# Kernel optimization log

Measured on AMD Instinct MI355X. Metric: run time of the kernel, lower is better.

## Reference

```python
import jax, jax.numpy as jnp
import numpy as np

B, T, H = 64, 512, 256
D = 2 * H            # input dim to slot LSTM (bidirectional encoder repr)
MAX_SLOTS = 64       # max slot spans kept per sentence
MAX_LEN = 8          # max tokens per span
N_SLOT_TYPES = 64


def _pack_spans(bio):
    """Segment BIO tags into spans: each span = B token + following I tokens.
    Returns token index table [B, MAX_SLOTS, MAX_LEN] and validity mask."""
    bsz, t = bio.shape
    bmask = bio == 1
    imask = bio == 2
    sid = jnp.cumsum(bmask.astype(jnp.int32), axis=1) - 1      # span id per token
    valid = (bmask | imask) & (sid >= 0)
    cs = jnp.cumsum(valid.astype(jnp.int32), axis=1)           # running count of span tokens
    bi = jnp.arange(bsz)[:, None]
    # cs value at each span's B token (overflow spans dumped into slot MAX_SLOTS)
    sid_b = jnp.where(bmask & (sid < MAX_SLOTS), sid, MAX_SLOTS)
    start = jnp.zeros((bsz, MAX_SLOTS + 1), jnp.int32).at[bi, sid_b].set(cs)[:, :MAX_SLOTS]
    sid_c = jnp.clip(sid, 0, MAX_SLOTS - 1)
    rank = cs - jnp.take_along_axis(start, sid_c, axis=1)      # position within span (B token -> 0)
    ok = valid & (sid < MAX_SLOTS) & (rank < MAX_LEN)
    s_idx = jnp.where(ok, sid_c, MAX_SLOTS)
    r_idx = jnp.where(ok, rank, MAX_LEN)
    tpos = jnp.broadcast_to(jnp.arange(t, dtype=jnp.int32), (bsz, t))
    tok = jnp.zeros((bsz, MAX_SLOTS + 1, MAX_LEN + 1), jnp.int32).at[bi, s_idx, r_idx].set(tpos)
    vm = jnp.zeros((bsz, MAX_SLOTS + 1, MAX_LEN + 1), bool).at[bi, s_idx, r_idx].set(True)
    return tok[:, :MAX_SLOTS, :MAX_LEN], vm[:, :MAX_SLOTS, :MAX_LEN]


def _lstm(x, Wih, Whh, b):
    """Unidirectional LSTM. x: [N, L, D] -> outputs [N, L, H] (torch gate order i,f,g,o)."""
    xg = jnp.einsum('nld,gd->nlg', x, Wih) + b                 # [N, L, 4H]
    n, l, _ = xg.shape
    h0 = jnp.zeros((n, Whh.shape[1]), x.dtype)

    def step(carry, xt):
        h, c = carry
        g = xt + h @ Whh.T
        i, f, gg, o = jnp.split(g, 4, axis=-1)
        c = jax.nn.sigmoid(f) * c + jax.nn.sigmoid(i) * jnp.tanh(gg)
        h = jax.nn.sigmoid(o) * jnp.tanh(c)
        return (h, c), h

    _, hs = jax.lax.scan(step, (h0, h0), jnp.swapaxes(xg, 0, 1))
    return jnp.swapaxes(hs, 0, 1)


def reference(lstm_repr, W_ih_f, W_hh_f, b_f, W_ih_b, W_hh_b, b_b, slot_emb, bio):
    tok, vm = _pack_spans(bio)                                  # [B,MS,ML], [B,MS,ML]
    bi = jnp.arange(lstm_repr.shape[0])[:, None, None]
    spans = lstm_repr[bi, tok]                                  # [B,MS,ML,D]
    lens = vm.sum(-1)                                           # [B,MS]
    # reverse each span within its valid length (padding stays at the end)
    pos = jnp.arange(MAX_LEN)
    rpos = lens[..., None] - 1 - pos
    ridx = jnp.where(rpos >= 0, rpos, 0)
    spans_rev = jnp.take_along_axis(spans, ridx[..., None], axis=2)
    ms = MAX_SLOTS
    xf = spans.reshape(-1, MAX_LEN, D)
    xb = spans_rev.reshape(-1, MAX_LEN, D)
    m = vm.reshape(-1, MAX_LEN, 1).astype(lstm_repr.dtype)
    hf = _lstm(xf, W_ih_f, W_hh_f, b_f)                         # [B*MS, ML, H]
    hb = _lstm(xb, W_ih_b, W_hh_b, b_b)
    pooled = jnp.concatenate([(hf * m).sum(1), (hb * m).sum(1)], axis=-1)  # sum-pool over span
    pooled = pooled.reshape(lstm_repr.shape[0], ms, 2 * H)
    scores = jnp.einsum('bsh,kh->bsk', pooled, slot_emb)        # [B,MS,n_slot_types]
    scores = scores * (lens > 0)[..., None]
    return scores


def setup_inputs() -> dict:
    key = jax.random.key(0)
    ks = jax.random.split(key, 9)
    s = 0.05
    return {
        'lstm_repr': jax.random.normal(ks[0], (B, T, D), jnp.float32),
        'W_ih_f': jax.random.normal(ks[1], (4 * H, D), jnp.float32) * s,
        'W_hh_f': jax.random.normal(ks[2], (4 * H, H), jnp.float32) * s,
        'b_f': jax.random.normal(ks[3], (4 * H,), jnp.float32) * s,
        'W_ih_b': jax.random.normal(ks[4], (4 * H, D), jnp.float32) * s,
        'W_hh_b': jax.random.normal(ks[5], (4 * H, H), jnp.float32) * s,
        'b_b': jax.random.normal(ks[6], (4 * H,), jnp.float32) * s,
        'slot_emb': jax.random.normal(ks[7], (N_SLOT_TYPES, 2 * H), jnp.float32) * s,
        'bio': jax.random.randint(ks[8], (B, T), 0, 3, dtype=jnp.int32),
    }
```

## Files before the change

### kernel.cpp

```cpp
#include <hip/hip_runtime.h>
#include <hip/hip_bf16.h>
#include <stdint.h>

#define B_ 64
#define T_ 512
#define H_ 256
#define D_ 512
#define MS_ 64
#define ML_ 8
#define NST_ 64

typedef unsigned short u16;
typedef __bf16 bf8 __attribute__((ext_vector_type(8)));
typedef float f4 __attribute__((ext_vector_type(4)));

__device__ __forceinline__ u16 f2bf(float f) {
    unsigned u = __builtin_bit_cast(unsigned, f);
    u += 0x7fffu + ((u >> 16) & 1u);
    return (u16)(u >> 16);
}
__device__ __forceinline__ float bf2f(u16 v) {
    return __builtin_bit_cast(float, (unsigned)v << 16);
}
__device__ __forceinline__ float sigm(float x) { return 1.f / (1.f + __expf(-x)); }


__global__ __launch_bounds__(512) void pack_spans2(const int* __restrict__ bio,
                                                   int* __restrict__ tok,
                                                   int* __restrict__ lenb) {
    __shared__ int wsum[8];
    __shared__ int start_s[64];
    __shared__ int len_s[64];
    int b = blockIdx.x;
    int t = threadIdx.x;
    int lane = t & 63, w = t >> 6;
    int v = bio[b * T_ + t];
    int bm = (v == 1);
    int im = (v == 2);
    if (t < 64) len_s[t] = 0;

    int x = bm;
#pragma unroll
    for (int off = 1; off < 64; off <<= 1) {
        int y = __shfl_up(x, off, 64);
        if (lane >= off) x += y;
    }
    if (lane == 63) wsum[w] = x;
    __syncthreads();
    int wof = 0;
    for (int i = 0; i < w; ++i) wof += wsum[i];
    int sid = x + wof - 1;
    int valid = ((bm | im) && sid >= 0) ? 1 : 0;
    __syncthreads();

    x = valid;
#pragma unroll
    for (int off = 1; off < 64; off <<= 1) {
        int y = __shfl_up(x, off, 64);
        if (lane >= off) x += y;
    }
    if (lane == 63) wsum[w] = x;
    __syncthreads();
    wof = 0;
    for (int i = 0; i < w; ++i) wof += wsum[i];
    int cs = x + wof;

    if (bm && sid < MS_) start_s[sid] = cs;
    __syncthreads();

    if (valid && sid < MS_) {
        int rank = cs - start_s[sid];
        if (rank < ML_) {
            tok[(b * MS_ + sid) * ML_ + rank] = t;
            atomicAdd(&len_s[sid], 1);
        }
    }
    __syncthreads();
    if (t < 64) lenb[b * MS_ + t] = len_s[t];
}

__global__ __launch_bounds__(256) void prep(
        const float* __restrict__ wihf, const float* __restrict__ whhf,
        const float* __restrict__ wihb, const float* __restrict__ whhb,
        const float* __restrict__ bf, const float* __restrict__ bb,
        u16* __restrict__ wcx, u16* __restrict__ wch, float* __restrict__ bc,
        const float* __restrict__ repr, const int* __restrict__ tok,
        const int* __restrict__ lenb,
        int* __restrict__ lists, int* __restrict__ counts, u16* __restrict__ xg) {
    int bid = blockIdx.x, gsz = gridDim.x, tid = threadIdx.x;
    if (bid == 0) {
        __shared__ int wsum[4];
        int lane = tid & 63, w = tid >> 6;
        int len[16];
#pragma unroll
        for (int i = 0; i < 16; ++i) len[i] = lenb[tid * 16 + i];
        for (int p = 0; p < ML_; ++p) {
            int c = 0;
#pragma unroll
            for (int i = 0; i < 16; ++i) c += (len[i] > p) ? 1 : 0;
            int x = c;
#pragma unroll
            for (int off = 1; off < 64; off <<= 1) {
                int y = __shfl_up(x, off, 64);
                if (lane >= off) x += y;
            }
            if (lane == 63) wsum[w] = x;
            __syncthreads();
            int wof = 0;
            for (int i = 0; i < w; ++i) wof += wsum[i];
            int pos = wof + x - c;
#pragma unroll
            for (int i = 0; i < 16; ++i)
                if (len[i] > p) lists[p * 4096 + pos++] = tid * 16 + i;
            if (tid == 255) counts[p] = pos;
            __syncthreads();
        }
        return;
    }
    int b1 = bid - 1, g1 = gsz - 1;
    for (int ch = b1; ch < 6152; ch += g1) {
        int i = ch * 256 + tid;
        if (i < 1572864) {
            int dir = i / 786432;
            int rem = i - dir * 786432;
            int n = rem / 768;
            int k = rem - n * 768;
            int nn = n & 63, c = n >> 6;
            int orig = (nn >> 4) * 256 + c * 16 + (nn & 15);
            if (k < 512) {
                const float* wih = dir ? wihb : wihf;
                wcx[((size_t)dir * 1024 + n) * 512 + k] = f2bf(wih[orig * 512 + k]);
            } else {
                const float* whh = dir ? whhb : whhf;
                wch[((size_t)dir * 1024 + n) * 256 + (k - 512)] =
                    f2bf(whh[orig * 256 + (k - 512)]);
            }
        } else if (i < 1574912) {
            int i2 = i - 1572864;
            int dir = i2 >> 10;
            int n = i2 & 1023;
            int nn = n & 63, c = n >> 6;
            int orig = (nn >> 4) * 256 + c * 16 + (nn & 15);
            bc[i2] = (dir ? bb : bf)[orig];
        }
    }
    for (int gq = b1; gq < 8192; gq += g1) {
        int sr = gq * 4 + (tid >> 6);
        int i = tid & 63;
        int span = sr >> 3, rank = sr & 7;
        if (rank < lenb[span]) {
            int t = tok[sr];
            int b = span >> 6;
            const float4* src = (const float4*)(repr + (size_t)(b * T_ + t) * D_);
            ushort4* dst = (ushort4*)(xg + (size_t)sr * D_);
            float4 v0 = src[i * 2], v1 = src[i * 2 + 1];
            ushort4 o0, o1;
            o0.x = f2bf(v0.x); o0.y = f2bf(v0.y); o0.z = f2bf(v0.z); o0.w = f2bf(v0.w);
            o1.x = f2bf(v1.x); o1.y = f2bf(v1.y); o1.z = f2bf(v1.z); o1.w = f2bf(v1.w);
            dst[i * 2] = o0; dst[i * 2 + 1] = o1;
        }
    }
}

__global__ __launch_bounds__(256) void xgk(const u16* __restrict__ xg,
                                           const u16* __restrict__ wcx,
                                           const float* __restrict__ bc,
                                           const int* __restrict__ lenb,
                                           const int* __restrict__ lists,
                                           const int* __restrict__ counts,
                                           u16* __restrict__ xgates,
                                           float* __restrict__ cbuf,
                                           u16* __restrict__ h1,
                                           float* __restrict__ pooled) {
    __shared__ __align__(16) u16 As[64 * 72];
    __shared__ __align__(16) u16 Bs[64 * 72];
    __shared__ unsigned xoffs[64];
    __shared__ int spans_s[64];
    int tid = threadIdx.x;
    int lane = tid & 63;
    int w16 = (tid >> 6) * 16;
    int mr = lane & 15;
    int q = lane >> 4;
    int q8 = q * 8;

    int S = 0;
#pragma unroll
    for (int pp = 0; pp < 8; ++pp) S += (counts[pp] + 63) >> 6;
    int S2 = 2 * S;

    int it = blockIdx.x;
    int qq = it >> 7, rem = it & 127, xs = rem >> 3, r8 = rem & 7;
    int g = qq * 8 + r8;
    if (g >= S2) return;
    int dir = (g >= S) ? 1 : 0;
    int gg = dir ? g - S : g;
    int p = 0;
#pragma unroll
    for (int pp = 0; pp < 7; ++pp) {
        int nbp = (counts[pp] + 63) >> 6;
        bool adv = (p == pp) && (gg >= nbp);
        if (adv) { gg -= nbp; p = pp + 1; }
    }
    int rbk = gg;
    int cnt = counts[p];
    int base = rbk * 64;

    if (tid < 64) {
        unsigned xo = 0;
        int span = 0;
        int idx = base + tid;
        if (idx < cnt) {
            span = lists[p * 4096 + idx];
            int L = lenb[span];
            int rank = dir ? (L - 1 - p) : p;
            xo = (unsigned)(span * ML_ + rank) * D_;
        }
        xoffs[tid] = xo;
        spans_s[tid] = span;
    }
    __syncthreads();

    int n0 = xs * 64;
    const u16* wb = wcx + (size_t)dir * 1024 * 512;
    f4 acc[4];
    f4 zed = {0.f, 0.f, 0.f, 0.f};
#pragma unroll
    for (int i = 0; i < 4; ++i) acc[i] = zed;

    for (int kt = 0; kt < 8; ++kt) {
#pragma unroll
        for (int i = 0; i < 2; ++i) {
            int c = tid + i * 256;
            int row = c >> 3;
            int cc = (c & 7) * 8;
            *(uint4*)&As[row * 72 + cc] =
                *(const uint4*)(xg + xoffs[row] + kt * 64 + cc);
            *(uint4*)&Bs[row * 72 + cc] =
                *(const uint4*)(wb + (size_t)(n0 + row) * 512 + kt * 64 + cc);
        }
        __syncthreads();
#pragma unroll
        for (int kk = 0; kk < 64; kk += 32) {
            bf8 af = *(const bf8*)&As[(w16 + mr) * 72 + kk + q8];
#pragma unroll
            for (int nt = 0; nt < 4; ++nt) {
                bf8 bg = *(const bf8*)&Bs[(nt * 16 + mr) * 72 + kk + q8];
                acc[nt] = __builtin_amdgcn_mfma_f32_16x16x32_bf16(af, bg, acc[nt], 0, 0, 0);
            }
        }
        __syncthreads();
    }

    float tf[16];
#pragma unroll
    for (int nt = 0; nt < 4; ++nt)
#pragma unroll
        for (int r = 0; r < 4; ++r) {
            int n = n0 + nt * 16 + mr;
            tf[nt * 4 + r] = acc[nt][r] + bc[dir * 1024 + n];
        }

    if (p == 0) {
        int j = xs * 16 + mr;
#pragma unroll
        for (int r = 0; r < 4; ++r) {
            int m = w16 + q * 4 + r;
            if (base + m < cnt) {
                int span = spans_s[m];
                float gi = tf[0 + r], gg2 = tf[8 + r], go = tf[12 + r];
                float cn = sigm(gi) * tanhf(gg2);
                float h = sigm(go) * tanhf(cn);
                int si = (dir * 4096 + span) * H_ + j;
                cbuf[si] = cn;
                h1[si] = f2bf(h);
                pooled[span * 512 + dir * H_ + j] = h;
            }
        }
    } else {
        int y = (dir * 8 + p) * 64 + rbk;
        u16 tmp[16];
#pragma unroll
        for (int i = 0; i < 16; ++i) tmp[i] = f2bf(tf[i]);
        size_t off = ((size_t)(y * 16 + xs) * 256 + tid) * 16;
        *(uint4*)&xgates[off] = *(const uint4*)tmp;
        *(uint4*)&xgates[off + 8] = *(const uint4*)(tmp + 8);
    }
}

__global__ __launch_bounds__(256) void stepk(const u16* __restrict__ xgates,
                                             const u16* __restrict__ hin,
                                             u16* __restrict__ hout,
                                             const u16* __restrict__ wch,
                                             const int* __restrict__ lists,
                                             const int* __restrict__ counts,
                                             float* __restrict__ cbuf,
                                             float* __restrict__ pooled, int p) {
    __shared__ __align__(16) u16 As[64 * 264];
    __shared__ __align__(16) u16 Bs[64 * 264];
    __shared__ unsigned hoffs[64];
    __shared__ int spans_s[64];
    int tid = threadIdx.x;
    int lane = tid & 63;
    int w16 = (tid >> 6) * 16;
    int mr = lane & 15;
    int q = lane >> 4;
    int q8 = q * 8;
    int cnt = counts[p];
    int nbp = (cnt + 63) >> 6;
    int S2 = 2 * nbp;

    int it = blockIdx.x;
    int g = it >> 4, xs = it & 15;
    if (g >= S2) return;
    int dir = (g >= nbp) ? 1 : 0;
    int rbk = dir ? g - nbp : g;
    int base = rbk * 64;

    if (tid < 64) {
        int span = 0;
        int idx = base + tid;
        if (idx < cnt) span = lists[p * 4096 + idx];
        spans_s[tid] = span;
        hoffs[tid] = (unsigned)(dir * 4096 + span) * H_;
    }
    __syncthreads();

    int n0 = xs * 64;
    const u16* wb = wch + (size_t)dir * 1024 * 256;
    int y = (dir * 8 + p) * 64 + rbk;
    u16 tmp[16];
    {
        const uint4* sx = (const uint4*)(xgates + ((size_t)(y * 16 + xs) * 256 + tid) * 16);
        ((uint4*)tmp)[0] = sx[0];
        ((uint4*)tmp)[1] = sx[1];
    }
    f4 acc[4];
#pragma unroll
    for (int nt = 0; nt < 4; ++nt)
#pragma unroll
        for (int r = 0; r < 4; ++r) acc[nt][r] = bf2f(tmp[nt * 4 + r]);

#pragma unroll
    for (int i = 0; i < 8; ++i) {
        int c = tid + i * 256;
        int row = c >> 5;
        int cc = (c & 31) * 8;
        *(uint4*)&As[row * 264 + cc] = *(const uint4*)(hin + hoffs[row] + cc);
        *(uint4*)&Bs[row * 264 + cc] =
            *(const uint4*)(wb + (size_t)(n0 + row) * 256 + cc);
    }
    __syncthreads();

#pragma unroll
    for (int kk = 0; kk < 256; kk += 32) {
        bf8 af = *(const bf8*)&As[(w16 + mr) * 264 + kk + q8];
#pragma unroll
        for (int nt = 0; nt < 4; ++nt) {
            bf8 bg = *(const bf8*)&Bs[(nt * 16 + mr) * 264 + kk + q8];
            acc[nt] = __builtin_amdgcn_mfma_f32_16x16x32_bf16(af, bg, acc[nt], 0, 0, 0);
        }
    }

#pragma unroll
    for (int r = 0; r < 4; ++r) {
        int m = w16 + q * 4 + r;
        if (base + m < cnt) {
            int span = spans_s[m];
            int j = xs * 16 + mr;
            float gi = acc[0][r], gf = acc[1][r], gg = acc[2][r], go = acc[3][r];
            int si = (dir * 4096 + span) * H_ + j;
            float c = cbuf[si];
            float cn = sigm(gf) * c + sigm(gi) * tanhf(gg);
            float h = sigm(go) * tanhf(cn);
            cbuf[si] = cn;
            hout[si] = f2bf(h);
            pooled[span * 512 + dir * H_ + j] += h;
        }
    }
}

__global__ __launch_bounds__(256) void scoresk(const float* __restrict__ pooled,
                                               const float* __restrict__ emb,
                                               const int* __restrict__ lenb,
                                               float* __restrict__ out) {
    __shared__ __align__(16) u16 As[64 * 72];
    __shared__ __align__(16) u16 Bs[64 * 72];
    int g = blockIdx.x;
    int tid = threadIdx.x;
    int lane = tid & 63;
    int w16 = (tid >> 6) * 16;
    int mr = lane & 15;
    int q = lane >> 4;
    int q8 = q * 8;

    f4 acc[4];
    f4 zed = {0.f, 0.f, 0.f, 0.f};
#pragma unroll
    for (int i = 0; i < 4; ++i) acc[i] = zed;

    for (int kt = 0; kt < 8; ++kt) {
#pragma unroll
        for (int i = 0; i < 2; ++i) {
            int c = tid + i * 256;
            int row = c >> 3;
            int cc = (c & 7) * 8;
            const float4* a =
                (const float4*)(pooled + (size_t)(g * 64 + row) * 512 + kt * 64 + cc);
            float4 v0 = a[0], v1 = a[1];
            ushort4 o0, o1;
            o0.x = f2bf(v0.x); o0.y = f2bf(v0.y); o0.z = f2bf(v0.z); o0.w = f2bf(v0.w);
            o1.x = f2bf(v1.x); o1.y = f2bf(v1.y); o1.z = f2bf(v1.z); o1.w = f2bf(v1.w);
            *(ushort4*)&As[row * 72 + cc] = o0;
            *(ushort4*)&As[row * 72 + cc + 4] = o1;
            const float4* b = (const float4*)(emb + (size_t)row * 512 + kt * 64 + cc);
            float4 w0 = b[0], w1 = b[1];
            ushort4 p0, p1;
            p0.x = f2bf(w0.x); p0.y = f2bf(w0.y); p0.z = f2bf(w0.z); p0.w = f2bf(w0.w);
            p1.x = f2bf(w1.x); p1.y = f2bf(w1.y); p1.z = f2bf(w1.z); p1.w = f2bf(w1.w);
            *(ushort4*)&Bs[row * 72 + cc] = p0;
            *(ushort4*)&Bs[row * 72 + cc + 4] = p1;
        }
        __syncthreads();
#pragma unroll
        for (int kk = 0; kk < 64; kk += 32) {
            bf8 af = *(const bf8*)&As[(w16 + mr) * 72 + kk + q8];
#pragma unroll
            for (int nt = 0; nt < 4; ++nt) {
                bf8 bg = *(const bf8*)&Bs[(nt * 16 + mr) * 72 + kk + q8];
                acc[nt] = __builtin_amdgcn_mfma_f32_16x16x32_bf16(af, bg, acc[nt], 0, 0, 0);
            }
        }
        __syncthreads();
    }

#pragma unroll
    for (int r = 0; r < 4; ++r) {
        int m = g * 64 + w16 + q * 4 + r;
        int ln = lenb[m];
#pragma unroll
        for (int nt = 0; nt < 4; ++nt) {
            int n = nt * 16 + mr;
            out[(size_t)m * 64 + n] = (ln > 0) ? acc[nt][r] : 0.f;
        }
    }
}


extern "C" void kernel_launch(void* const* d_in, const int* in_sizes, int n_in,
                              void* d_out, int out_size, void* d_ws, size_t ws_size,
                              hipStream_t stream) {
    const float* lstm_repr = (const float*)d_in[0];
    const float* W_ih_f = (const float*)d_in[1];
    const float* W_hh_f = (const float*)d_in[2];
    const float* b_f    = (const float*)d_in[3];
    const float* W_ih_b = (const float*)d_in[4];
    const float* W_hh_b = (const float*)d_in[5];
    const float* b_b    = (const float*)d_in[6];
    const float* slot_emb = (const float*)d_in[7];
    const int* bio      = (const int*)d_in[8];
    float* out = (float*)d_out;

    char* ws = (char*)d_ws;
    u16*  xg     = (u16*)(ws + 0);
    u16*  xgates = (u16*)(ws + 33554432);
    u16*  wcx    = (u16*)(ws + 167772160);
    u16*  wch    = (u16*)(ws + 169869312);
    float* bc    = (float*)(ws + 170917888);
    int*  tok    = (int*)(ws + 170926080);
    int*  lenb   = (int*)(ws + 171057152);
    int*  lists  = (int*)(ws + 171073536);
    int*  counts = (int*)(ws + 171204608);
    float* pooled= (float*)(ws + 171204864);
    float* cbuf  = (float*)(ws + 179593472);
    u16*  h0     = (u16*)(ws + 187982080);
    u16*  h1     = (u16*)(ws + 192176384);

    pack_spans2<<<64, 512, 0, stream>>>(bio, tok, lenb);
    prep<<<2048, 256, 0, stream>>>(W_ih_f, W_hh_f, W_ih_b, W_hh_b, b_f, b_b,
                                   wcx, wch, bc, lstm_repr, tok, lenb,
                                   lists, counts, xg);
    xgk<<<16384, 256, 0, stream>>>(xg, wcx, bc, lenb, lists, counts, xgates,
                                   cbuf, h1, pooled);
    for (int p = 1; p < 8; ++p) {
        const u16* hin = (p & 1) ? h1 : h0;
        u16* hout = (p & 1) ? h0 : h1;
        stepk<<<2048, 256, 0, stream>>>(xgates, hin, hout, wch, lists, counts,
                                        cbuf, pooled, p);
    }
    scoresk<<<64, 256, 0, stream>>>(pooled, slot_emb, lenb, out);
}
```

Baseline: 243.3 us.

## Fuse seven recurrent step launches into one persistent kernel with length-sorted spans

Spans are now sorted by descending length into one master list, so every timestep's active set is a prefix of that list. The seven per-step launches are replaced by a single kernel of 128 blocks. Each block owns 64 spans and one direction, keeps h in LDS across steps, and loops over all 16 gate column slices, double-buffering the W_hh tiles. This removes the launch overhead and the global round trips for h, but the grid shrinks from 2048 blocks to 128, so parallelism drops and each block reloads all of W_hh at every step.

```diff
diff --git a/kernel.cpp b/kernel.cpp
--- a/kernel.cpp
+++ b/kernel.cpp
@@ -86,7 +86,7 @@
         u16* __restrict__ wcx, u16* __restrict__ wch, float* __restrict__ bc,
         const float* __restrict__ repr, const int* __restrict__ tok,
         const int* __restrict__ lenb,
-        int* __restrict__ lists, int* __restrict__ counts, u16* __restrict__ xg) {
+        int* __restrict__ master, int* __restrict__ counts, u16* __restrict__ xg) {
     int bid = blockIdx.x, gsz = gridDim.x, tid = threadIdx.x;
     if (bid == 0) {
         __shared__ int wsum[4];
@@ -94,25 +94,28 @@
         int len[16];
 #pragma unroll
         for (int i = 0; i < 16; ++i) len[i] = lenb[tid * 16 + i];
-        for (int p = 0; p < ML_; ++p) {
+        int off = 0;
+        for (int L = 8; L >= 1; --L) {
             int c = 0;
 #pragma unroll
-            for (int i = 0; i < 16; ++i) c += (len[i] > p) ? 1 : 0;
+            for (int i = 0; i < 16; ++i) c += (len[i] == L) ? 1 : 0;
             int x = c;
 #pragma unroll
-            for (int off = 1; off < 64; off <<= 1) {
-                int y = __shfl_up(x, off, 64);
-                if (lane >= off) x += y;
+            for (int o = 1; o < 64; o <<= 1) {
+                int y = __shfl_up(x, o, 64);
+                if (lane >= o) x += y;
             }
             if (lane == 63) wsum[w] = x;
             __syncthreads();
             int wof = 0;
             for (int i = 0; i < w; ++i) wof += wsum[i];
-            int pos = wof + x - c;
+            int tot = wsum[0] + wsum[1] + wsum[2] + wsum[3];
+            int pos = off + wof + x - c;
 #pragma unroll
             for (int i = 0; i < 16; ++i)
-                if (len[i] > p) lists[p * 4096 + pos++] = tid * 16 + i;
-            if (tid == 255) counts[p] = pos;
+                if (len[i] == L) master[pos++] = tid * 16 + i;
+            off += tot;
+            if (tid == 0) counts[L - 1] = off;
             __syncthreads();
         }
         return;
@@ -166,7 +169,7 @@
                                            const u16* __restrict__ wcx,
                                            const float* __restrict__ bc,
                                            const int* __restrict__ lenb,
-                                           const int* __restrict__ lists,
+                                           const int* __restrict__ master,
                                            const int* __restrict__ counts,
                                            u16* __restrict__ xgates,
                                            float* __restrict__ cbuf,
@@ -210,7 +213,7 @@
         int span = 0;
         int idx = base + tid;
         if (idx < cnt) {
-            span = lists[p * 4096 + idx];
+            span = master[idx];
             int L = lenb[span];
             int rank = dir ? (L - 1 - p) : p;
             xo = (unsigned)(span * ML_ + rank) * D_;
@@ -287,17 +290,15 @@
     }
 }
 
-__global__ __launch_bounds__(256) void stepk(const u16* __restrict__ xgates,
-                                             const u16* __restrict__ hin,
-                                             u16* __restrict__ hout,
-                                             const u16* __restrict__ wch,
-                                             const int* __restrict__ lists,
-                                             const int* __restrict__ counts,
-                                             float* __restrict__ cbuf,
-                                             float* __restrict__ pooled, int p) {
-    __shared__ __align__(16) u16 As[64 * 264];
-    __shared__ __align__(16) u16 Bs[64 * 264];
-    __shared__ unsigned hoffs[64];
+__global__ __launch_bounds__(256) void fsteps(const u16* __restrict__ xgates,
+                                              const u16* __restrict__ h1,
+                                              const u16* __restrict__ wch,
+                                              const int* __restrict__ master,
+                                              const int* __restrict__ counts,
+                                              float* __restrict__ cbuf,
+                                              float* __restrict__ pooled) {
+    __shared__ __align__(16) u16 Abuf[2][64 * 264];
+    __shared__ __align__(16) u16 Bbuf[2][64 * 264];
     __shared__ int spans_s[64];
     int tid = threadIdx.x;
     int lane = tid & 63;
@@ -305,77 +306,119 @@
     int mr = lane & 15;
     int q = lane >> 4;
     int q8 = q * 8;
-    int cnt = counts[p];
-    int nbp = (cnt + 63) >> 6;
-    int S2 = 2 * nbp;
-
-    int it = blockIdx.x;
-    int g = it >> 4, xs = it & 15;
-    if (g >= S2) return;
-    int dir = (g >= nbp) ? 1 : 0;
-    int rbk = dir ? g - nbp : g;
+    int dir = blockIdx.x >> 6;
+    int rbk = blockIdx.x & 63;
     int base = rbk * 64;
+    if (base >= counts[1]) return;
+    int cnt0 = counts[0];
 
     if (tid < 64) {
         int span = 0;
         int idx = base + tid;
-        if (idx < cnt) span = lists[p * 4096 + idx];
+        if (idx < cnt0) span = master[idx];
         spans_s[tid] = span;
-        hoffs[tid] = (unsigned)(dir * 4096 + span) * H_;
-    }
-    __syncthreads();
-
-    int n0 = xs * 64;
-    const u16* wb = wch + (size_t)dir * 1024 * 256;
-    int y = (dir * 8 + p) * 64 + rbk;
-    u16 tmp[16];
-    {
-        const uint4* sx = (const uint4*)(xgates + ((size_t)(y * 16 + xs) * 256 + tid) * 16);
-        ((uint4*)tmp)[0] = sx[0];
-        ((uint4*)tmp)[1] = sx[1];
-    }
-    f4 acc[4];
-#pragma unroll
-    for (int nt = 0; nt < 4; ++nt)
-#pragma unroll
-        for (int r = 0; r < 4; ++r) acc[nt][r] = bf2f(tmp[nt * 4 + r]);
+    }
+    __syncthreads();
 
 #pragma unroll
     for (int i = 0; i < 8; ++i) {
         int c = tid + i * 256;
         int row = c >> 5;
         int cc = (c & 31) * 8;
-        *(uint4*)&As[row * 264 + cc] = *(const uint4*)(hin + hoffs[row] + cc);
-        *(uint4*)&Bs[row * 264 + cc] =
-            *(const uint4*)(wb + (size_t)(n0 + row) * 256 + cc);
-    }
-    __syncthreads();
-
-#pragma unroll
-    for (int kk = 0; kk < 256; kk += 32) {
-        bf8 af = *(const bf8*)&As[(w16 + mr) * 264 + kk + q8];
-#pragma unroll
-        for (int nt = 0; nt < 4; ++nt) {
-            bf8 bg = *(const bf8*)&Bs[(nt * 16 + mr) * 264 + kk + q8];
-            acc[nt] = __builtin_amdgcn_mfma_f32_16x16x32_bf16(af, bg, acc[nt], 0, 0, 0);
-        }
-    }
-
-#pragma unroll
-    for (int r = 0; r < 4; ++r) {
-        int m = w16 + q * 4 + r;
-        if (base + m < cnt) {
-            int span = spans_s[m];
+        unsigned ho = (unsigned)(dir * 4096 + spans_s[row]) * H_;
+        *(uint4*)&Abuf[0][row * 264 + cc] = *(const uint4*)(h1 + ho + cc);
+    }
+
+    const u16* wb = wch + (size_t)dir * 1024 * 256;
+    int pc = 0;
+
+    for (int p = 1; p < 8; ++p) {
+        int cnt = counts[p];
+        if (base >= cnt) break;
+        int y = (dir * 8 + p) * 64 + rbk;
+
+        uint4 breg[8];
+#pragma unroll
+        for (int i = 0; i < 8; ++i) {
+            int c = tid + i * 256;
+            breg[i] = *(const uint4*)(wb + (size_t)(c >> 5) * 256 + (c & 31) * 8);
+        }
+#pragma unroll
+        for (int i = 0; i < 8; ++i) {
+            int c = tid + i * 256;
+            *(uint4*)&Bbuf[0][(c >> 5) * 264 + (c & 31) * 8] = breg[i];
+        }
+#pragma unroll
+        for (int i = 0; i < 8; ++i) {
+            int c = tid + i * 256;
+            breg[i] = *(const uint4*)(wb + (size_t)(64 + (c >> 5)) * 256 + (c & 31) * 8);
+        }
+        uint4 xreg[2];
+        {
+            const uint4* sx = (const uint4*)(xgates + ((size_t)(y * 16) * 256 + tid) * 16);
+            xreg[0] = sx[0]; xreg[1] = sx[1];
+        }
+        __syncthreads();
+
+#pragma unroll
+        for (int xs = 0; xs < 16; ++xs) {
+            u16 tmp[16];
+            *(uint4*)tmp = xreg[0];
+            *(uint4*)(tmp + 8) = xreg[1];
+            f4 acc[4];
+#pragma unroll
+            for (int nt = 0; nt < 4; ++nt)
+#pragma unroll
+                for (int r = 0; r < 4; ++r) acc[nt][r] = bf2f(tmp[nt * 4 + r]);
+            if (xs < 15) {
+                const uint4* sx =
+                    (const uint4*)(xgates + ((size_t)(y * 16 + xs + 1) * 256 + tid) * 16);
+                xreg[0] = sx[0]; xreg[1] = sx[1];
+            }
+#pragma unroll
+            for (int kk = 0; kk < 256; kk += 32) {
+                bf8 af = *(const bf8*)&Abuf[pc][(w16 + mr) * 264 + kk + q8];
+#pragma unroll
+                for (int nt = 0; nt < 4; ++nt) {
+                    bf8 bg = *(const bf8*)&Bbuf[xs & 1][(nt * 16 + mr) * 264 + kk + q8];
+                    acc[nt] =
+                        __builtin_amdgcn_mfma_f32_16x16x32_bf16(af, bg, acc[nt], 0, 0, 0);
+                }
+            }
+            if (xs < 15) {
+#pragma unroll
+                for (int i = 0; i < 8; ++i) {
+                    int c = tid + i * 256;
+                    *(uint4*)&Bbuf[(xs + 1) & 1][(c >> 5) * 264 + (c & 31) * 8] = breg[i];
+                }
+                if (xs < 14) {
+#pragma unroll
+                    for (int i = 0; i < 8; ++i) {
+                        int c = tid + i * 256;
+                        breg[i] = *(const uint4*)(wb + (size_t)((xs + 2) * 64 + (c >> 5)) * 256
+                                                  + (c & 31) * 8);
+                    }
+                }
+            }
             int j = xs * 16 + mr;
-            float gi = acc[0][r], gf = acc[1][r], gg = acc[2][r], go = acc[3][r];
-            int si = (dir * 4096 + span) * H_ + j;
-            float c = cbuf[si];
-            float cn = sigm(gf) * c + sigm(gi) * tanhf(gg);
-            float h = sigm(go) * tanhf(cn);
-            cbuf[si] = cn;
-            hout[si] = f2bf(h);
-            pooled[span * 512 + dir * H_ + j] += h;
-        }
+#pragma unroll
+            for (int r = 0; r < 4; ++r) {
+                int m = w16 + q * 4 + r;
+                if (base + m < cnt) {
+                    int span = spans_s[m];
+                    float gi = acc[0][r], gf = acc[1][r], gg = acc[2][r], go = acc[3][r];
+                    int si = (dir * 4096 + span) * H_ + j;
+                    float c = cbuf[si];
+                    float cn = sigm(gf) * c + sigm(gi) * tanhf(gg);
+                    float h = sigm(go) * tanhf(cn);
+                    cbuf[si] = cn;
+                    Abuf[pc ^ 1][m * 264 + j] = f2bf(h);
+                    pooled[span * 512 + dir * H_ + j] += h;
+                }
+            }
+            __syncthreads();
+        }
+        pc ^= 1;
     }
 }
 
@@ -468,24 +511,20 @@
     float* bc    = (float*)(ws + 170917888);
     int*  tok    = (int*)(ws + 170926080);
     int*  lenb   = (int*)(ws + 171057152);
-    int*  lists  = (int*)(ws + 171073536);
+    int*  master = (int*)(ws + 171073536);
     int*  counts = (int*)(ws + 171204608);
     float* pooled= (float*)(ws + 171204864);
     float* cbuf  = (float*)(ws + 179593472);
     u16*  h0     = (u16*)(ws + 187982080);
     u16*  h1     = (u16*)(ws + 192176384);
+    (void)h0;
 
     pack_spans2<<<64, 512, 0, stream>>>(bio, tok, lenb);
     prep<<<2048, 256, 0, stream>>>(W_ih_f, W_hh_f, W_ih_b, W_hh_b, b_f, b_b,
                                    wcx, wch, bc, lstm_repr, tok, lenb,
-                                   lists, counts, xg);
-    xgk<<<16384, 256, 0, stream>>>(xg, wcx, bc, lenb, lists, counts, xgates,
+                                   master, counts, xg);
+    xgk<<<16384, 256, 0, stream>>>(xg, wcx, bc, lenb, master, counts, xgates,
                                    cbuf, h1, pooled);
-    for (int p = 1; p < 8; ++p) {
-        const u16* hin = (p & 1) ? h1 : h0;
-        u16* hout = (p & 1) ? h0 : h1;
-        stepk<<<2048, 256, 0, stream>>>(xgates, hin, hout, wch, lists, counts,
-                                        cbuf, pooled, p);
-    }
+    fsteps<<<128, 256, 0, stream>>>(xgates, h1, wch, master, counts, cbuf, pooled);
     scoresk<<<64, 256, 0, stream>>>(pooled, slot_emb, lenb, out);
 }
```

Measured after the change: 746.0 us. +206.7%, slower.
